# Optimization experiments

Measured on AMD Instinct MI355X. Metric: run time of the kernel, lower is better.

## Reference

```python
import jax, jax.numpy as jnp
import numpy as np

B, S, D, H = 4, 2048, 768, 12
HD = D // H  # head_dim = 64

def setup_inputs() -> dict:
    key = jax.random.key(0)
    k1, k2, k3 = jax.random.split(key, 3)
    scale = 0.02
    return {
        "x": jax.random.normal(k1, (B, S, D), dtype=jnp.float32),
        "w_qkv": jax.random.normal(k2, (D, 3 * D), dtype=jnp.float32) * scale,
        "b_qkv": jnp.zeros((3 * D,), dtype=jnp.float32),
        "w_proj": jax.random.normal(k3, (D, D), dtype=jnp.float32) * scale,
        "b_proj": jnp.zeros((D,), dtype=jnp.float32),
    }

def reference(x, w_qkv, b_qkv, w_proj, b_proj):
    b, s, d = x.shape
    hd = d // H
    attn_scale = hd ** -0.5
    qkv = x @ w_qkv + b_qkv                      # [b, s, 3d]
    qkv = qkv.reshape(b, s, 3, H, hd)
    q, k, v = jnp.moveaxis(qkv, 2, 0)            # each [b, s, H, hd]
    q = q.transpose(0, 2, 1, 3)                  # [b, H, s, hd]
    k = k.transpose(0, 2, 1, 3)
    v = v.transpose(0, 2, 1, 3)
    attn = jnp.einsum("bhqd,bhkd->bhqk", q, k) * attn_scale  # [b, H, s, s]
    causal = jnp.tril(jnp.ones((s, s), dtype=bool))
    attn = jnp.where(causal[None, None], attn, -jnp.inf)
    attn = jax.nn.softmax(attn, axis=-1)
    out = jnp.einsum("bhqk,bhkd->bhqd", attn, v)  # [b, H, s, hd]
    out = out.transpose(0, 2, 1, 3).reshape(b, s, d)
    return out @ w_proj + b_proj
```

## Files before the change

### kernel.cpp

```cpp
#include <hip/hip_runtime.h>
#include <hip/hip_bf16.h>
#include <cstdint>

typedef __bf16 bf16_t;
typedef __bf16 bf16x4 __attribute__((ext_vector_type(4)));
typedef __bf16 bf16x8 __attribute__((ext_vector_type(8)));
typedef float floatx4 __attribute__((ext_vector_type(4)));
typedef float floatx16 __attribute__((ext_vector_type(16)));
typedef unsigned int u32x4 __attribute__((ext_vector_type(4)));

#define NB 4
#define NH 12
#define SEQ 2048
#define DM 768
#define LOG2E 1.44269504088896340736f

__device__ __forceinline__ void gload_lds16(const bf16_t* g, bf16_t* l) {
  auto gp = reinterpret_cast<const __attribute__((address_space(1))) uint32_t*>(
      reinterpret_cast<uintptr_t>(g));
  auto lp = reinterpret_cast<__attribute__((address_space(3))) uint32_t*>(
      reinterpret_cast<uintptr_t>(l));
  __builtin_amdgcn_global_load_lds(gp, lp, 16, 0, 0);
}

__device__ __forceinline__ unsigned int pack2(float a, float b) {
  bf16_t x = (bf16_t)a, y = (bf16_t)b;
  unsigned short ux = __builtin_bit_cast(unsigned short, x);
  unsigned short uy = __builtin_bit_cast(unsigned short, y);
  return (unsigned int)ux | ((unsigned int)uy << 16);
}

__global__ __launch_bounds__(256) void prep_kernel(
    const float* __restrict__ x, bf16_t* __restrict__ xb,
    const float* __restrict__ wqkv, bf16_t* __restrict__ wqkvT,
    const float* __restrict__ wproj, bf16_t* __restrict__ wprojT) {
  const int bid = blockIdx.x;
  const int tid = threadIdx.x;
  if (bid < 6144) {
    int i = (bid * 256 + tid) * 4;
    float4 v = *(const float4*)(x + i);
    bf16x4 hh;
    hh[0] = (bf16_t)v.x; hh[1] = (bf16_t)v.y; hh[2] = (bf16_t)v.z; hh[3] = (bf16_t)v.w;
    *(bf16x4*)(xb + i) = hh;
    return;
  }
  const float* in;
  bf16_t* out;
  int N, nb, kb;
  if (bid < 7872) {
    int t = bid - 6144;
    in = wqkv; out = wqkvT; N = 2304;
    nb = (t % 72) * 32; kb = (t / 72) * 32;
  } else {
    int t = bid - 7872;
    in = wproj; out = wprojT; N = 768;
    nb = (t % 24) * 32; kb = (t / 24) * 32;
  }
  const int K = 768;
  __shared__ float tile[32][33];
  int tx = tid & 31, ty = tid >> 5;
#pragma unroll
  for (int r = ty; r < 32; r += 8)
    tile[r][tx] = in[(size_t)(kb + r) * N + nb + tx];
  __syncthreads();
#pragma unroll
  for (int r = ty; r < 32; r += 8)
    out[(size_t)(nb + r) * K + kb + tx] = (bf16_t)tile[tx][r];
}

__global__ __launch_bounds__(256) void gemm_qkv_kernel(
    const bf16_t* __restrict__ A, const bf16_t* __restrict__ BT,
    const float* __restrict__ bias,
    bf16_t* __restrict__ Qo, bf16_t* __restrict__ Ko, bf16_t* __restrict__ Vo) {
  const int K = 768;
  __shared__ __align__(16) bf16_t As[128][32];
  __shared__ __align__(16) bf16_t Bs[128][32];
  const int m0 = blockIdx.x * 128, n0 = blockIdx.y * 128;
  const int tid = threadIdx.x;
  const int w = tid >> 6, lane = tid & 63, quad = lane >> 4, l16 = lane & 15;
  const int wm = w >> 1, wn = w & 1;
  const int ldrow = w * 32;
  const int grow = lane >> 2;
  const int gcol = (lane & 3) * 8;

  floatx4 acc[4][4];
#pragma unroll
  for (int mt = 0; mt < 4; mt++)
#pragma unroll
    for (int nt = 0; nt < 4; nt++) acc[mt][nt] = (floatx4)(0.f);

  const bf16_t* ga0 = A + (size_t)(m0 + ldrow) * K;
  const bf16_t* gb0 = BT + (size_t)(n0 + ldrow) * K;

  for (int k0 = 0; k0 < K; k0 += 32) {
    __syncthreads();
    gload_lds16(ga0 + (size_t)grow * K + k0 + gcol,        &As[ldrow][0]);
    gload_lds16(ga0 + (size_t)(grow + 16) * K + k0 + gcol, &As[ldrow + 16][0]);
    gload_lds16(gb0 + (size_t)grow * K + k0 + gcol,        &Bs[ldrow][0]);
    gload_lds16(gb0 + (size_t)(grow + 16) * K + k0 + gcol, &Bs[ldrow + 16][0]);
    __syncthreads();
    bf16x8 af[4], bfr[4];
#pragma unroll
    for (int mt = 0; mt < 4; mt++)
      af[mt] = *(const bf16x8*)&As[wm * 64 + mt * 16 + l16][quad * 8];
#pragma unroll
    for (int nt = 0; nt < 4; nt++)
      bfr[nt] = *(const bf16x8*)&Bs[wn * 64 + nt * 16 + l16][quad * 8];
#pragma unroll
    for (int mt = 0; mt < 4; mt++)
#pragma unroll
      for (int nt = 0; nt < 4; nt++)
        acc[mt][nt] = __builtin_amdgcn_mfma_f32_16x16x32_bf16(af[mt], bfr[nt], acc[mt][nt], 0, 0, 0);
  }

  const int which = n0 / 768;
  const int rem0 = n0 % 768;
  bf16_t* dst = which == 0 ? Qo : (which == 1 ? Ko : Vo);
  const float qscale = which == 0 ? (0.125f * LOG2E) : 1.0f;
#pragma unroll
  for (int nt = 0; nt < 4; nt++) {
    const int cc = wn * 64 + nt * 16 + l16;
    const int rem = rem0 + cc;
    const int h = rem >> 6, hd = rem & 63;
    const float bv = bias[n0 + cc];
#pragma unroll
    for (int mt = 0; mt < 4; mt++)
#pragma unroll
      for (int r = 0; r < 4; r++) {
        const int gr = m0 + wm * 64 + mt * 16 + quad * 4 + r;
        const int bb = gr >> 11, s = gr & 2047;
        const float val = (acc[mt][nt][r] + bv) * qscale;
        dst[((size_t)((bb * NH + h) * SEQ + s)) * 64 + hd] = (bf16_t)val;
      }
  }
}

__global__ __launch_bounds__(256) void vtrans_kernel(const bf16_t* __restrict__ V,
                                                     bf16_t* __restrict__ Vt) {
  __shared__ bf16_t tile[64][66];
  int bh = blockIdx.y, s0 = blockIdx.x * 64;
  int tid = threadIdx.x;
  int r = tid >> 4, c4 = (tid & 15) * 4;
  const bf16_t* src = V + (size_t)bh * SEQ * 64;
#pragma unroll
  for (int rr = r; rr < 64; rr += 16)
    *(bf16x4*)&tile[rr][c4] = *(const bf16x4*)&src[(size_t)(s0 + rr) * 64 + c4];
  __syncthreads();
  bf16_t* dst = Vt + (size_t)bh * 64 * SEQ;
#pragma unroll
  for (int hd = r; hd < 64; hd += 16) {
    bf16x4 o;
    o[0] = tile[c4 + 0][hd]; o[1] = tile[c4 + 1][hd];
    o[2] = tile[c4 + 2][hd]; o[3] = tile[c4 + 3][hd];
    *(bf16x4*)&dst[(size_t)hd * SEQ + s0 + c4] = o;
  }
}

__global__ __launch_bounds__(512, 4) void attn_kernel(
    const bf16_t* __restrict__ Q, const bf16_t* __restrict__ Kg,
    const bf16_t* __restrict__ Vt, bf16_t* __restrict__ Out) {
  __shared__ __align__(16) bf16_t Ks[3][64 * 64];
  __shared__ __align__(16) bf16_t Vs[3][64 * 64];
  const int tid = threadIdx.x;
  const int w = tid >> 6, lane = tid & 63;
  const int l31 = lane & 31, hi = lane >> 5;
  const int bh = blockIdx.x;
  const int b = bh / NH, h = bh % NH;
  const int qt = (int)(gridDim.y - 1) - (int)blockIdx.y;
  const int r0 = qt * 256 + w * 32;
  const int qrow = r0 + l31;
  const bf16_t* Qp = Q + (size_t)bh * SEQ * 64;
  const bf16_t* Kp = Kg + (size_t)bh * SEQ * 64;
  const bf16_t* Vp = Vt + (size_t)bh * 64 * SEQ;

  bf16x8 qf[4];
#pragma unroll
  for (int kc = 0; kc < 4; kc++)
    qf[kc] = *(const bf16x8*)&Qp[(size_t)qrow * 64 + kc * 16 + hi * 8];

  bf16x8 ones;
#pragma unroll
  for (int j = 0; j < 8; j++) ones[j] = (bf16_t)1.0f;

  float m_i = -1e30f;
  floatx16 accT[2];
  accT[0] = (floatx16)(0.f);
  accT[1] = (floatx16)(0.f);
  floatx16 zl = (floatx16)(0.f);

  const int nt_w = (r0 >> 6) + 1;
  const int ntmax = 4 * qt + 4;

  const int srow = tid >> 3;
  const int scolb = ((tid & 7) ^ (srow & 7)) << 4;

  auto stage = [&](int buf, int kt) {
    const int kbase = kt * 64;
    gload_lds16(Kp + (size_t)(kbase + srow) * 64 + (scolb >> 1), &Ks[buf][w * 512]);
    gload_lds16(Vp + (size_t)srow * SEQ + kbase + (scolb >> 1), &Vs[buf][w * 512]);
  };

  const int swz = (l31 & 7) << 4;

  stage(0, 0);

  int cur = 0;
  for (int kt = 0; kt < ntmax; kt++) {
    const int nxt = (cur == 2) ? 0 : cur + 1;
    if (kt + 1 < ntmax) {
      stage(nxt, kt + 1);
      asm volatile("s_waitcnt vmcnt(2)" ::: "memory");
    } else {
      asm volatile("s_waitcnt vmcnt(0)" ::: "memory");
    }
    __builtin_amdgcn_s_barrier();

    if (kt < nt_w) {
      const int kbase = kt * 64;
      const bf16_t* Kb = Ks[cur];
      const bf16_t* Vb = Vs[cur];
      floatx16 st[2];
#pragma unroll
      for (int kt2 = 0; kt2 < 2; kt2++) {
        const int row = kt2 * 32 + l31;
        floatx16 z = (floatx16)(0.f);
#pragma unroll
        for (int kc = 0; kc < 4; kc++) {
          bf16x8 kfr = *(const bf16x8*)&Kb[row * 64 + (((kc * 32 + hi * 16) ^ swz) >> 1)];
          z = __builtin_amdgcn_mfma_f32_32x32x16_bf16(kfr, qf[kc], z, 0, 0, 0);
        }
        st[kt2] = z;
      }
      if (kt == nt_w - 1) {
#pragma unroll
        for (int kt2 = 0; kt2 < 2; kt2++)
#pragma unroll
          for (int r = 0; r < 16; r++) {
            int key = kbase + kt2 * 32 + (r & 3) + 8 * (r >> 2) + 4 * hi;
            if (key > qrow) st[kt2][r] = -1e30f;
          }
      }
      float mloc = -1e30f;
#pragma unroll
      for (int kt2 = 0; kt2 < 2; kt2++)
#pragma unroll
        for (int r = 0; r < 16; r++) mloc = fmaxf(mloc, st[kt2][r]);
      mloc = fmaxf(mloc, __shfl_xor(mloc, 32));
      if (!__all((int)(mloc - m_i <= 8.f))) {
        const float mnew = fmaxf(m_i, mloc);
        const float al = __builtin_amdgcn_exp2f(m_i - mnew);
        m_i = mnew;
#pragma unroll
        for (int r = 0; r < 16; r++) zl[r] *= al;
#pragma unroll
        for (int dt = 0; dt < 2; dt++)
#pragma unroll
          for (int r = 0; r < 16; r++) accT[dt][r] *= al;
      }
#pragma unroll
      for (int kt2 = 0; kt2 < 2; kt2++)
#pragma unroll
        for (int r = 0; r < 16; r++)
          st[kt2][r] = __builtin_amdgcn_exp2f(st[kt2][r] - m_i);
#pragma unroll
      for (int kt2 = 0; kt2 < 2; kt2++) {
        unsigned int wds[8];
#pragma unroll
        for (int j = 0; j < 8; j++) wds[j] = pack2(st[kt2][2 * j], st[kt2][2 * j + 1]);
        unsigned int x0 = (unsigned int)__shfl_xor((int)(hi ? wds[0] : wds[2]), 32);
        unsigned int x1 = (unsigned int)__shfl_xor((int)(hi ? wds[1] : wds[3]), 32);
        unsigned int x2 = (unsigned int)__shfl_xor((int)(hi ? wds[4] : wds[6]), 32);
        unsigned int x3 = (unsigned int)__shfl_xor((int)(hi ? wds[5] : wds[7]), 32);
        u32x4 f0 = hi ? (u32x4){x0, x1, wds[2], wds[3]} : (u32x4){wds[0], wds[1], x0, x1};
        u32x4 f1 = hi ? (u32x4){x2, x3, wds[6], wds[7]} : (u32x4){wds[4], wds[5], x2, x3};
        bf16x8 pf0 = __builtin_bit_cast(bf16x8, f0);
        bf16x8 pf1 = __builtin_bit_cast(bf16x8, f1);
        zl = __builtin_amdgcn_mfma_f32_32x32x16_bf16(ones, pf0, zl, 0, 0, 0);
        zl = __builtin_amdgcn_mfma_f32_32x32x16_bf16(ones, pf1, zl, 0, 0, 0);
#pragma unroll
        for (int dt = 0; dt < 2; dt++) {
          const int vrow = dt * 32 + l31;
          bf16x8 v0 = *(const bf16x8*)&Vb[vrow * 64 + (((kt2 * 64 + hi * 16) ^ swz) >> 1)];
          bf16x8 v1 = *(const bf16x8*)&Vb[vrow * 64 + (((kt2 * 64 + 32 + hi * 16) ^ swz) >> 1)];
          accT[dt] = __builtin_amdgcn_mfma_f32_32x32x16_bf16(v0, pf0, accT[dt], 0, 0, 0);
          accT[dt] = __builtin_amdgcn_mfma_f32_32x32x16_bf16(v1, pf1, accT[dt], 0, 0, 0);
        }
      }
    }
    cur = nxt;
  }

  const float inv_l = 1.0f / zl[0];
#pragma unroll
  for (int dt = 0; dt < 2; dt++)
#pragma unroll
    for (int g = 0; g < 4; g++) {
      bf16x4 o;
#pragma unroll
      for (int j = 0; j < 4; j++) o[j] = (bf16_t)(accT[dt][4 * g + j] * inv_l);
      int d = dt * 32 + 8 * g + 4 * hi;
      *(bf16x4*)&Out[((size_t)(b * SEQ + qrow)) * DM + h * 64 + d] = o;
    }
}

__global__ __launch_bounds__(256) void gemm_proj_kernel(
    const bf16_t* __restrict__ A, const bf16_t* __restrict__ BT,
    const float* __restrict__ bias, float* __restrict__ out) {
  const int K = 768;
  __shared__ __align__(16) bf16_t As[128][32];
  __shared__ __align__(16) bf16_t Bs[128][32];
  const int m0 = blockIdx.x * 128, n0 = blockIdx.y * 128;
  const int tid = threadIdx.x;
  const int w = tid >> 6, lane = tid & 63, quad = lane >> 4, l16 = lane & 15;
  const int wm = w >> 1, wn = w & 1;
  const int ldrow = w * 32;
  const int grow = lane >> 2;
  const int gcol = (lane & 3) * 8;

  floatx4 acc[4][4];
#pragma unroll
  for (int mt = 0; mt < 4; mt++)
#pragma unroll
    for (int nt = 0; nt < 4; nt++) acc[mt][nt] = (floatx4)(0.f);

  const bf16_t* ga0 = A + (size_t)(m0 + ldrow) * K;
  const bf16_t* gb0 = BT + (size_t)(n0 + ldrow) * K;

  for (int k0 = 0; k0 < K; k0 += 32) {
    __syncthreads();
    gload_lds16(ga0 + (size_t)grow * K + k0 + gcol,        &As[ldrow][0]);
    gload_lds16(ga0 + (size_t)(grow + 16) * K + k0 + gcol, &As[ldrow + 16][0]);
    gload_lds16(gb0 + (size_t)grow * K + k0 + gcol,        &Bs[ldrow][0]);
    gload_lds16(gb0 + (size_t)(grow + 16) * K + k0 + gcol, &Bs[ldrow + 16][0]);
    __syncthreads();
    bf16x8 af[4], bfr[4];
#pragma unroll
    for (int mt = 0; mt < 4; mt++)
      af[mt] = *(const bf16x8*)&As[wm * 64 + mt * 16 + l16][quad * 8];
#pragma unroll
    for (int nt = 0; nt < 4; nt++)
      bfr[nt] = *(const bf16x8*)&Bs[wn * 64 + nt * 16 + l16][quad * 8];
#pragma unroll
    for (int mt = 0; mt < 4; mt++)
#pragma unroll
      for (int nt = 0; nt < 4; nt++)
        acc[mt][nt] = __builtin_amdgcn_mfma_f32_16x16x32_bf16(af[mt], bfr[nt], acc[mt][nt], 0, 0, 0);
  }

#pragma unroll
  for (int nt = 0; nt < 4; nt++) {
    const int gc = n0 + wn * 64 + nt * 16 + l16;
    const float bv = bias[gc];
#pragma unroll
    for (int mt = 0; mt < 4; mt++)
#pragma unroll
      for (int r = 0; r < 4; r++) {
        const int gr = m0 + wm * 64 + mt * 16 + quad * 4 + r;
        out[(size_t)gr * 768 + gc] = acc[mt][nt][r] + bv;
      }
  }
}

extern "C" void kernel_launch(void* const* d_in, const int* in_sizes, int n_in,
                              void* d_out, int out_size, void* d_ws, size_t ws_size,
                              hipStream_t stream) {
  const float* x      = (const float*)d_in[0];
  const float* w_qkv  = (const float*)d_in[1];
  const float* b_qkv  = (const float*)d_in[2];
  const float* w_proj = (const float*)d_in[3];
  const float* b_proj = (const float*)d_in[4];
  float* out = (float*)d_out;
  char* ws = (char*)d_ws;

  bf16_t* xb     = (bf16_t*)(ws + 0);
  bf16_t* wqkvT  = (bf16_t*)(ws + 12582912);
  bf16_t* wprojT = (bf16_t*)(ws + 16121856);
  bf16_t* q      = (bf16_t*)(ws + 17301504);
  bf16_t* k      = (bf16_t*)(ws + 29884416);
  bf16_t* v      = (bf16_t*)(ws + 42467328);
  bf16_t* ao     = (bf16_t*)(ws + 55050240);
  bf16_t* vt     = xb;

  prep_kernel<<<8448, 256, 0, stream>>>(x, xb, w_qkv, wqkvT, w_proj, wprojT);
  gemm_qkv_kernel<<<dim3(64, 18), 256, 0, stream>>>(xb, wqkvT, b_qkv, q, k, v);
  vtrans_kernel<<<dim3(32, 48), 256, 0, stream>>>(v, vt);
  attn_kernel<<<dim3(48, 8), 512, 0, stream>>>(q, k, vt, ao);
  gemm_proj_kernel<<<dim3(64, 6), 256, 0, stream>>>(ao, wprojT, b_proj, out);
}
```

Baseline: 214.5 us.

## Triple-buffer GEMM K-loop loads and halve attention query tile per block

```diff
diff --git a/kernel.cpp b/kernel.cpp
--- a/kernel.cpp
+++ b/kernel.cpp
@@ -73,8 +73,9 @@
     const float* __restrict__ bias,
     bf16_t* __restrict__ Qo, bf16_t* __restrict__ Ko, bf16_t* __restrict__ Vo) {
   const int K = 768;
-  __shared__ __align__(16) bf16_t As[128][32];
-  __shared__ __align__(16) bf16_t Bs[128][32];
+  const int NT = 24;
+  __shared__ __align__(16) bf16_t As[3][128 * 32];
+  __shared__ __align__(16) bf16_t Bs[3][128 * 32];
   const int m0 = blockIdx.x * 128, n0 = blockIdx.y * 128;
   const int tid = threadIdx.x;
   const int w = tid >> 6, lane = tid & 63, quad = lane >> 4, l16 = lane & 15;
@@ -92,25 +93,38 @@
   const bf16_t* ga0 = A + (size_t)(m0 + ldrow) * K;
   const bf16_t* gb0 = BT + (size_t)(n0 + ldrow) * K;
 
-  for (int k0 = 0; k0 < K; k0 += 32) {
-    __syncthreads();
-    gload_lds16(ga0 + (size_t)grow * K + k0 + gcol,        &As[ldrow][0]);
-    gload_lds16(ga0 + (size_t)(grow + 16) * K + k0 + gcol, &As[ldrow + 16][0]);
-    gload_lds16(gb0 + (size_t)grow * K + k0 + gcol,        &Bs[ldrow][0]);
-    gload_lds16(gb0 + (size_t)(grow + 16) * K + k0 + gcol, &Bs[ldrow + 16][0]);
-    __syncthreads();
+  auto stage = [&](int buf, int k0) {
+    gload_lds16(ga0 + (size_t)grow * K + k0 + gcol,        &As[buf][ldrow * 32]);
+    gload_lds16(ga0 + (size_t)(grow + 16) * K + k0 + gcol, &As[buf][(ldrow + 16) * 32]);
+    gload_lds16(gb0 + (size_t)grow * K + k0 + gcol,        &Bs[buf][ldrow * 32]);
+    gload_lds16(gb0 + (size_t)(grow + 16) * K + k0 + gcol, &Bs[buf][(ldrow + 16) * 32]);
+  };
+
+  stage(0, 0);
+  int cur = 0;
+  for (int t = 0; t < NT; t++) {
+    const int nxt = (cur == 2) ? 0 : cur + 1;
+    if (t + 1 < NT) {
+      stage(nxt, (t + 1) * 32);
+      asm volatile("s_waitcnt vmcnt(4)" ::: "memory");
+    } else {
+      asm volatile("s_waitcnt vmcnt(0)" ::: "memory");
+    }
+    __builtin_amdgcn_s_barrier();
+
     bf16x8 af[4], bfr[4];
 #pragma unroll
     for (int mt = 0; mt < 4; mt++)
-      af[mt] = *(const bf16x8*)&As[wm * 64 + mt * 16 + l16][quad * 8];
+      af[mt] = *(const bf16x8*)&As[cur][(wm * 64 + mt * 16 + l16) * 32 + quad * 8];
 #pragma unroll
     for (int nt = 0; nt < 4; nt++)
-      bfr[nt] = *(const bf16x8*)&Bs[wn * 64 + nt * 16 + l16][quad * 8];
+      bfr[nt] = *(const bf16x8*)&Bs[cur][(wn * 64 + nt * 16 + l16) * 32 + quad * 8];
 #pragma unroll
     for (int mt = 0; mt < 4; mt++)
 #pragma unroll
       for (int nt = 0; nt < 4; nt++)
         acc[mt][nt] = __builtin_amdgcn_mfma_f32_16x16x32_bf16(af[mt], bfr[nt], acc[mt][nt], 0, 0, 0);
+    cur = nxt;
   }
 
   const int which = n0 / 768;
@@ -156,7 +170,7 @@
   }
 }
 
-__global__ __launch_bounds__(512, 4) void attn_kernel(
+__global__ __launch_bounds__(256, 3) void attn_kernel(
     const bf16_t* __restrict__ Q, const bf16_t* __restrict__ Kg,
     const bf16_t* __restrict__ Vt, bf16_t* __restrict__ Out) {
   __shared__ __align__(16) bf16_t Ks[3][64 * 64];
@@ -167,7 +181,7 @@
   const int bh = blockIdx.x;
   const int b = bh / NH, h = bh % NH;
   const int qt = (int)(gridDim.y - 1) - (int)blockIdx.y;
-  const int r0 = qt * 256 + w * 32;
+  const int r0 = qt * 128 + w * 32;
   const int qrow = r0 + l31;
   const bf16_t* Qp = Q + (size_t)bh * SEQ * 64;
   const bf16_t* Kp = Kg + (size_t)bh * SEQ * 64;
@@ -189,15 +203,26 @@
   floatx16 zl = (floatx16)(0.f);
 
   const int nt_w = (r0 >> 6) + 1;
-  const int ntmax = 4 * qt + 4;
-
-  const int srow = tid >> 3;
-  const int scolb = ((tid & 7) ^ (srow & 7)) << 4;
+  const int ntmax = 2 * qt + 2;
+
+  int srow[2], scolb[2];
+#pragma unroll
+  for (int r = 0; r < 2; r++) {
+    int off = r * 4096 + w * 1024 + lane * 16;
+    int row = off >> 7;
+    srow[r] = row;
+    scolb[r] = (off & 127) ^ ((row & 7) << 4);
+  }
 
   auto stage = [&](int buf, int kt) {
     const int kbase = kt * 64;
-    gload_lds16(Kp + (size_t)(kbase + srow) * 64 + (scolb >> 1), &Ks[buf][w * 512]);
-    gload_lds16(Vp + (size_t)srow * SEQ + kbase + (scolb >> 1), &Vs[buf][w * 512]);
+#pragma unroll
+    for (int r = 0; r < 2; r++) {
+      gload_lds16(Kp + (size_t)(kbase + srow[r]) * 64 + (scolb[r] >> 1),
+                  &Ks[buf][r * 2048 + w * 512]);
+      gload_lds16(Vp + (size_t)srow[r] * SEQ + kbase + (scolb[r] >> 1),
+                  &Vs[buf][r * 2048 + w * 512]);
+    }
   };
 
   const int swz = (l31 & 7) << 4;
@@ -209,7 +234,7 @@
     const int nxt = (cur == 2) ? 0 : cur + 1;
     if (kt + 1 < ntmax) {
       stage(nxt, kt + 1);
-      asm volatile("s_waitcnt vmcnt(2)" ::: "memory");
+      asm volatile("s_waitcnt vmcnt(4)" ::: "memory");
     } else {
       asm volatile("s_waitcnt vmcnt(0)" ::: "memory");
     }
@@ -307,8 +332,9 @@
     const bf16_t* __restrict__ A, const bf16_t* __restrict__ BT,
     const float* __restrict__ bias, float* __restrict__ out) {
   const int K = 768;
-  __shared__ __align__(16) bf16_t As[128][32];
-  __shared__ __align__(16) bf16_t Bs[128][32];
+  const int NT = 24;
+  __shared__ __align__(16) bf16_t As[3][128 * 32];
+  __shared__ __align__(16) bf16_t Bs[3][128 * 32];
   const int m0 = blockIdx.x * 128, n0 = blockIdx.y * 128;
   const int tid = threadIdx.x;
   const int w = tid >> 6, lane = tid & 63, quad = lane >> 4, l16 = lane & 15;
@@ -326,25 +352,38 @@
   const bf16_t* ga0 = A + (size_t)(m0 + ldrow) * K;
   const bf16_t* gb0 = BT + (size_t)(n0 + ldrow) * K;
 
-  for (int k0 = 0; k0 < K; k0 += 32) {
-    __syncthreads();
-    gload_lds16(ga0 + (size_t)grow * K + k0 + gcol,        &As[ldrow][0]);
-    gload_lds16(ga0 + (size_t)(grow + 16) * K + k0 + gcol, &As[ldrow + 16][0]);
-    gload_lds16(gb0 + (size_t)grow * K + k0 + gcol,        &Bs[ldrow][0]);
-    gload_lds16(gb0 + (size_t)(grow + 16) * K + k0 + gcol, &Bs[ldrow + 16][0]);
-    __syncthreads();
+  auto stage = [&](int buf, int k0) {
+    gload_lds16(ga0 + (size_t)grow * K + k0 + gcol,        &As[buf][ldrow * 32]);
+    gload_lds16(ga0 + (size_t)(grow + 16) * K + k0 + gcol, &As[buf][(ldrow + 16) * 32]);
+    gload_lds16(gb0 + (size_t)grow * K + k0 + gcol,        &Bs[buf][ldrow * 32]);
+    gload_lds16(gb0 + (size_t)(grow + 16) * K + k0 + gcol, &Bs[buf][(ldrow + 16) * 32]);
+  };
+
+  stage(0, 0);
+  int cur = 0;
+  for (int t = 0; t < NT; t++) {
+    const int nxt = (cur == 2) ? 0 : cur + 1;
+    if (t + 1 < NT) {
+      stage(nxt, (t + 1) * 32);
+      asm volatile("s_waitcnt vmcnt(4)" ::: "memory");
+    } else {
+      asm volatile("s_waitcnt vmcnt(0)" ::: "memory");
+    }
+    __builtin_amdgcn_s_barrier();
+
     bf16x8 af[4], bfr[4];
 #pragma unroll
     for (int mt = 0; mt < 4; mt++)
-      af[mt] = *(const bf16x8*)&As[wm * 64 + mt * 16 + l16][quad * 8];
+      af[mt] = *(const bf16x8*)&As[cur][(wm * 64 + mt * 16 + l16) * 32 + quad * 8];
 #pragma unroll
     for (int nt = 0; nt < 4; nt++)
-      bfr[nt] = *(const bf16x8*)&Bs[wn * 64 + nt * 16 + l16][quad * 8];
+      bfr[nt] = *(const bf16x8*)&Bs[cur][(wn * 64 + nt * 16 + l16) * 32 + quad * 8];
 #pragma unroll
     for (int mt = 0; mt < 4; mt++)
 #pragma unroll
       for (int nt = 0; nt < 4; nt++)
         acc[mt][nt] = __builtin_amdgcn_mfma_f32_16x16x32_bf16(af[mt], bfr[nt], acc[mt][nt], 0, 0, 0);
+    cur = nxt;
   }
 
 #pragma unroll
@@ -384,6 +423,6 @@
   prep_kernel<<<8448, 256, 0, stream>>>(x, xb, w_qkv, wqkvT, w_proj, wprojT);
   gemm_qkv_kernel<<<dim3(64, 18), 256, 0, stream>>>(xb, wqkvT, b_qkv, q, k, v);
   vtrans_kernel<<<dim3(32, 48), 256, 0, stream>>>(v, vt);
-  attn_kernel<<<dim3(48, 8), 512, 0, stream>>>(q, k, vt, ao);
+  attn_kernel<<<dim3(48, 16), 256, 0, stream>>>(q, k, vt, ao);
   gemm_proj_kernel<<<dim3(64, 6), 256, 0, stream>>>(ao, wprojT, b_proj, out);
 }
```

After: 205.9 us. 1.04x faster.

## Fuse V transpose into QKV GEMM epilogue and shrink attention blocks to 64 query rows

Applied to the files above, without the earlier changes.

```diff
diff --git a/kernel.cpp b/kernel.cpp
--- a/kernel.cpp
+++ b/kernel.cpp
@@ -71,10 +71,11 @@
 __global__ __launch_bounds__(256) void gemm_qkv_kernel(
     const bf16_t* __restrict__ A, const bf16_t* __restrict__ BT,
     const float* __restrict__ bias,
-    bf16_t* __restrict__ Qo, bf16_t* __restrict__ Ko, bf16_t* __restrict__ Vo) {
+    bf16_t* __restrict__ Qo, bf16_t* __restrict__ Ko, bf16_t* __restrict__ Vto) {
   const int K = 768;
-  __shared__ __align__(16) bf16_t As[128][32];
-  __shared__ __align__(16) bf16_t Bs[128][32];
+  __shared__ __align__(16) bf16_t smem[128 * 136];
+  bf16_t* As = smem;
+  bf16_t* Bs = smem + 4096;
   const int m0 = blockIdx.x * 128, n0 = blockIdx.y * 128;
   const int tid = threadIdx.x;
   const int w = tid >> 6, lane = tid & 63, quad = lane >> 4, l16 = lane & 15;
@@ -94,18 +95,18 @@
 
   for (int k0 = 0; k0 < K; k0 += 32) {
     __syncthreads();
-    gload_lds16(ga0 + (size_t)grow * K + k0 + gcol,        &As[ldrow][0]);
-    gload_lds16(ga0 + (size_t)(grow + 16) * K + k0 + gcol, &As[ldrow + 16][0]);
-    gload_lds16(gb0 + (size_t)grow * K + k0 + gcol,        &Bs[ldrow][0]);
-    gload_lds16(gb0 + (size_t)(grow + 16) * K + k0 + gcol, &Bs[ldrow + 16][0]);
+    gload_lds16(ga0 + (size_t)grow * K + k0 + gcol,        &As[ldrow * 32]);
+    gload_lds16(ga0 + (size_t)(grow + 16) * K + k0 + gcol, &As[(ldrow + 16) * 32]);
+    gload_lds16(gb0 + (size_t)grow * K + k0 + gcol,        &Bs[ldrow * 32]);
+    gload_lds16(gb0 + (size_t)(grow + 16) * K + k0 + gcol, &Bs[(ldrow + 16) * 32]);
     __syncthreads();
     bf16x8 af[4], bfr[4];
 #pragma unroll
     for (int mt = 0; mt < 4; mt++)
-      af[mt] = *(const bf16x8*)&As[wm * 64 + mt * 16 + l16][quad * 8];
+      af[mt] = *(const bf16x8*)&As[(wm * 64 + mt * 16 + l16) * 32 + quad * 8];
 #pragma unroll
     for (int nt = 0; nt < 4; nt++)
-      bfr[nt] = *(const bf16x8*)&Bs[wn * 64 + nt * 16 + l16][quad * 8];
+      bfr[nt] = *(const bf16x8*)&Bs[(wn * 64 + nt * 16 + l16) * 32 + quad * 8];
 #pragma unroll
     for (int mt = 0; mt < 4; mt++)
 #pragma unroll
@@ -115,59 +116,64 @@
 
   const int which = n0 / 768;
   const int rem0 = n0 % 768;
-  bf16_t* dst = which == 0 ? Qo : (which == 1 ? Ko : Vo);
-  const float qscale = which == 0 ? (0.125f * LOG2E) : 1.0f;
-#pragma unroll
-  for (int nt = 0; nt < 4; nt++) {
-    const int cc = wn * 64 + nt * 16 + l16;
-    const int rem = rem0 + cc;
+  if (which < 2) {
+    bf16_t* dst = which == 0 ? Qo : Ko;
+    const float qscale = which == 0 ? (0.125f * LOG2E) : 1.0f;
+#pragma unroll
+    for (int nt = 0; nt < 4; nt++) {
+      const int cc = wn * 64 + nt * 16 + l16;
+      const int rem = rem0 + cc;
+      const int h = rem >> 6, hd = rem & 63;
+      const float bv = bias[n0 + cc];
+#pragma unroll
+      for (int mt = 0; mt < 4; mt++)
+#pragma unroll
+        for (int r = 0; r < 4; r++) {
+          const int gr = m0 + wm * 64 + mt * 16 + quad * 4 + r;
+          const int bb = gr >> 11, s = gr & 2047;
+          const float val = (acc[mt][nt][r] + bv) * qscale;
+          dst[((size_t)((bb * NH + h) * SEQ + s)) * 64 + hd] = (bf16_t)val;
+        }
+    }
+  } else {
+    __syncthreads();
+#pragma unroll
+    for (int nt = 0; nt < 4; nt++) {
+      const int c = wn * 64 + nt * 16 + l16;
+      const float bv = bias[n0 + c];
+#pragma unroll
+      for (int mt = 0; mt < 4; mt++)
+#pragma unroll
+        for (int r = 0; r < 4; r++) {
+          const int grl = wm * 64 + mt * 16 + quad * 4 + r;
+          smem[c * 136 + grl] = (bf16_t)(acc[mt][nt][r] + bv);
+        }
+    }
+    __syncthreads();
+    const int c = tid >> 1, half = tid & 1;
+    const int rem = rem0 + c;
     const int h = rem >> 6, hd = rem & 63;
-    const float bv = bias[n0 + cc];
-#pragma unroll
-    for (int mt = 0; mt < 4; mt++)
-#pragma unroll
-      for (int r = 0; r < 4; r++) {
-        const int gr = m0 + wm * 64 + mt * 16 + quad * 4 + r;
-        const int bb = gr >> 11, s = gr & 2047;
-        const float val = (acc[mt][nt][r] + bv) * qscale;
-        dst[((size_t)((bb * NH + h) * SEQ + s)) * 64 + hd] = (bf16_t)val;
-      }
-  }
-}
-
-__global__ __launch_bounds__(256) void vtrans_kernel(const bf16_t* __restrict__ V,
-                                                     bf16_t* __restrict__ Vt) {
-  __shared__ bf16_t tile[64][66];
-  int bh = blockIdx.y, s0 = blockIdx.x * 64;
-  int tid = threadIdx.x;
-  int r = tid >> 4, c4 = (tid & 15) * 4;
-  const bf16_t* src = V + (size_t)bh * SEQ * 64;
-#pragma unroll
-  for (int rr = r; rr < 64; rr += 16)
-    *(bf16x4*)&tile[rr][c4] = *(const bf16x4*)&src[(size_t)(s0 + rr) * 64 + c4];
-  __syncthreads();
-  bf16_t* dst = Vt + (size_t)bh * 64 * SEQ;
-#pragma unroll
-  for (int hd = r; hd < 64; hd += 16) {
-    bf16x4 o;
-    o[0] = tile[c4 + 0][hd]; o[1] = tile[c4 + 1][hd];
-    o[2] = tile[c4 + 2][hd]; o[3] = tile[c4 + 3][hd];
-    *(bf16x4*)&dst[(size_t)hd * SEQ + s0 + c4] = o;
-  }
-}
-
-__global__ __launch_bounds__(512, 4) void attn_kernel(
+    const int bb = m0 >> 11;
+    const int s0 = (m0 & 2047) + half * 64;
+    bf16_t* dstp = Vto + (((size_t)(bb * NH + h) * 64 + hd) << 11) + s0;
+#pragma unroll
+    for (int j = 0; j < 8; j++)
+      *(bf16x8*)(dstp + j * 8) = *(const bf16x8*)&smem[c * 136 + half * 64 + j * 8];
+  }
+}
+
+__global__ __launch_bounds__(128, 3) void attn_kernel(
     const bf16_t* __restrict__ Q, const bf16_t* __restrict__ Kg,
     const bf16_t* __restrict__ Vt, bf16_t* __restrict__ Out) {
-  __shared__ __align__(16) bf16_t Ks[3][64 * 64];
-  __shared__ __align__(16) bf16_t Vs[3][64 * 64];
+  __shared__ __align__(16) bf16_t Ks[2][64 * 64];
+  __shared__ __align__(16) bf16_t Vs[2][64 * 64];
   const int tid = threadIdx.x;
   const int w = tid >> 6, lane = tid & 63;
   const int l31 = lane & 31, hi = lane >> 5;
   const int bh = blockIdx.x;
   const int b = bh / NH, h = bh % NH;
   const int qt = (int)(gridDim.y - 1) - (int)blockIdx.y;
-  const int r0 = qt * 256 + w * 32;
+  const int r0 = qt * 64 + w * 32;
   const int qrow = r0 + l31;
   const bf16_t* Qp = Q + (size_t)bh * SEQ * 64;
   const bf16_t* Kp = Kg + (size_t)bh * SEQ * 64;
@@ -188,16 +194,26 @@
   accT[1] = (floatx16)(0.f);
   floatx16 zl = (floatx16)(0.f);
 
-  const int nt_w = (r0 >> 6) + 1;
-  const int ntmax = 4 * qt + 4;
-
-  const int srow = tid >> 3;
-  const int scolb = ((tid & 7) ^ (srow & 7)) << 4;
+  const int ntmax = qt + 1;
+
+  int srow[4], scolb[4];
+#pragma unroll
+  for (int r = 0; r < 4; r++) {
+    int off = r * 2048 + tid * 16;
+    int row = off >> 7;
+    srow[r] = row;
+    scolb[r] = (off & 127) ^ ((row & 7) << 4);
+  }
 
   auto stage = [&](int buf, int kt) {
     const int kbase = kt * 64;
-    gload_lds16(Kp + (size_t)(kbase + srow) * 64 + (scolb >> 1), &Ks[buf][w * 512]);
-    gload_lds16(Vp + (size_t)srow * SEQ + kbase + (scolb >> 1), &Vs[buf][w * 512]);
+#pragma unroll
+    for (int r = 0; r < 4; r++) {
+      gload_lds16(Kp + (size_t)(kbase + srow[r]) * 64 + (scolb[r] >> 1),
+                  &Ks[buf][r * 1024 + w * 512]);
+      gload_lds16(Vp + (size_t)srow[r] * SEQ + kbase + (scolb[r] >> 1),
+                  &Vs[buf][r * 1024 + w * 512]);
+    }
   };
 
   const int swz = (l31 & 7) << 4;
@@ -206,16 +222,15 @@
 
   int cur = 0;
   for (int kt = 0; kt < ntmax; kt++) {
-    const int nxt = (cur == 2) ? 0 : cur + 1;
     if (kt + 1 < ntmax) {
-      stage(nxt, kt + 1);
-      asm volatile("s_waitcnt vmcnt(2)" ::: "memory");
+      stage(cur ^ 1, kt + 1);
+      asm volatile("s_waitcnt vmcnt(8)" ::: "memory");
     } else {
       asm volatile("s_waitcnt vmcnt(0)" ::: "memory");
     }
     __builtin_amdgcn_s_barrier();
 
-    if (kt < nt_w) {
+    {
       const int kbase = kt * 64;
       const bf16_t* Kb = Ks[cur];
       const bf16_t* Vb = Vs[cur];
@@ -231,7 +246,7 @@
         }
         st[kt2] = z;
       }
-      if (kt == nt_w - 1) {
+      if (kt == ntmax - 1) {
 #pragma unroll
         for (int kt2 = 0; kt2 < 2; kt2++)
 #pragma unroll
@@ -287,7 +302,8 @@
         }
       }
     }
-    cur = nxt;
+    __builtin_amdgcn_s_barrier();
+    cur ^= 1;
   }
 
   const float inv_l = 1.0f / zl[0];
@@ -377,13 +393,11 @@
   bf16_t* wprojT = (bf16_t*)(ws + 16121856);
   bf16_t* q      = (bf16_t*)(ws + 17301504);
   bf16_t* k      = (bf16_t*)(ws + 29884416);
-  bf16_t* v      = (bf16_t*)(ws + 42467328);
+  bf16_t* vt     = (bf16_t*)(ws + 42467328);
   bf16_t* ao     = (bf16_t*)(ws + 55050240);
-  bf16_t* vt     = xb;
 
   prep_kernel<<<8448, 256, 0, stream>>>(x, xb, w_qkv, wqkvT, w_proj, wprojT);
-  gemm_qkv_kernel<<<dim3(64, 18), 256, 0, stream>>>(xb, wqkvT, b_qkv, q, k, v);
-  vtrans_kernel<<<dim3(32, 48), 256, 0, stream>>>(v, vt);
-  attn_kernel<<<dim3(48, 8), 512, 0, stream>>>(q, k, vt, ao);
+  gemm_qkv_kernel<<<dim3(64, 18), 256, 0, stream>>>(xb, wqkvT, b_qkv, q, k, vt);
+  attn_kernel<<<dim3(48, 32), 128, 0, stream>>>(q, k, vt, ao);
   gemm_proj_kernel<<<dim3(64, 6), 256, 0, stream>>>(ao, wprojT, b_proj, out);
 }
```

After: 219.2 us. 1.02x slower.

## Enlarge QKV GEMM tiles with double-buffered swizzled LDS; shrink attention blocks

Applied to the files above, without the earlier changes.

```diff
diff --git a/kernel.cpp b/kernel.cpp
--- a/kernel.cpp
+++ b/kernel.cpp
@@ -68,49 +68,97 @@
     out[(size_t)(nb + r) * K + kb + tx] = (bf16_t)tile[tx][r];
 }
 
-__global__ __launch_bounds__(256) void gemm_qkv_kernel(
+__global__ __launch_bounds__(512, 2) void gemm_qkv_kernel(
     const bf16_t* __restrict__ A, const bf16_t* __restrict__ BT,
     const float* __restrict__ bias,
     bf16_t* __restrict__ Qo, bf16_t* __restrict__ Ko, bf16_t* __restrict__ Vo) {
   const int K = 768;
-  __shared__ __align__(16) bf16_t As[128][32];
-  __shared__ __align__(16) bf16_t Bs[128][32];
-  const int m0 = blockIdx.x * 128, n0 = blockIdx.y * 128;
+  const int NKT = 12;
+  __shared__ __align__(16) bf16_t As[2][16384];
+  __shared__ __align__(16) bf16_t Bs[2][16384];
+  const int m0 = blockIdx.x * 256, n0 = blockIdx.y * 256;
   const int tid = threadIdx.x;
   const int w = tid >> 6, lane = tid & 63, quad = lane >> 4, l16 = lane & 15;
-  const int wm = w >> 1, wn = w & 1;
-  const int ldrow = w * 32;
-  const int grow = lane >> 2;
-  const int gcol = (lane & 3) * 8;
-
-  floatx4 acc[4][4];
-#pragma unroll
-  for (int mt = 0; mt < 4; mt++)
-#pragma unroll
-    for (int nt = 0; nt < 4; nt++) acc[mt][nt] = (floatx4)(0.f);
-
-  const bf16_t* ga0 = A + (size_t)(m0 + ldrow) * K;
-  const bf16_t* gb0 = BT + (size_t)(n0 + ldrow) * K;
-
-  for (int k0 = 0; k0 < K; k0 += 32) {
-    __syncthreads();
-    gload_lds16(ga0 + (size_t)grow * K + k0 + gcol,        &As[ldrow][0]);
-    gload_lds16(ga0 + (size_t)(grow + 16) * K + k0 + gcol, &As[ldrow + 16][0]);
-    gload_lds16(gb0 + (size_t)grow * K + k0 + gcol,        &Bs[ldrow][0]);
-    gload_lds16(gb0 + (size_t)(grow + 16) * K + k0 + gcol, &Bs[ldrow + 16][0]);
-    __syncthreads();
-    bf16x8 af[4], bfr[4];
-#pragma unroll
-    for (int mt = 0; mt < 4; mt++)
-      af[mt] = *(const bf16x8*)&As[wm * 64 + mt * 16 + l16][quad * 8];
-#pragma unroll
-    for (int nt = 0; nt < 4; nt++)
-      bfr[nt] = *(const bf16x8*)&Bs[wn * 64 + nt * 16 + l16][quad * 8];
-#pragma unroll
-    for (int mt = 0; mt < 4; mt++)
-#pragma unroll
-      for (int nt = 0; nt < 4; nt++)
-        acc[mt][nt] = __builtin_amdgcn_mfma_f32_16x16x32_bf16(af[mt], bfr[nt], acc[mt][nt], 0, 0, 0);
+  const int wm = w >> 2, wn = w & 3;
+  const int swz = (l16 & 7) << 4;
+
+  floatx4 acc[8][4];
+#pragma unroll
+  for (int m = 0; m < 8; m++)
+#pragma unroll
+    for (int n = 0; n < 4; n++) acc[m][n] = (floatx4)(0.f);
+
+  int srow[2], scol[2];
+#pragma unroll
+  for (int j = 0; j < 2; j++) {
+    int off = j * 8192 + tid * 16;
+    int row = off >> 7;
+    srow[j] = row;
+    scol[j] = (((off & 127) ^ ((row & 7) << 4)) >> 1);
+  }
+
+  auto stageA = [&](int d, int h, int kt) {
+#pragma unroll
+    for (int j = 0; j < 2; j++)
+      gload_lds16(A + (size_t)(m0 + h * 128 + srow[j]) * K + kt * 64 + scol[j],
+                  &As[d][h * 8192 + j * 4096 + w * 512]);
+  };
+  auto stageB = [&](int d, int h, int kt) {
+#pragma unroll
+    for (int j = 0; j < 2; j++)
+      gload_lds16(BT + (size_t)(n0 + h * 128 + srow[j]) * K + kt * 64 + scol[j],
+                  &Bs[d][h * 8192 + j * 4096 + w * 512]);
+  };
+
+  stageA(0, 0, 0); stageB(0, 0, 0); stageA(0, 1, 0); stageB(0, 1, 0);
+
+  for (int kt = 0; kt < NKT; kt++) {
+    const int d = kt & 1, nd = d ^ 1;
+    asm volatile("s_waitcnt vmcnt(0)" ::: "memory");
+    __builtin_amdgcn_s_barrier();
+
+    bf16x8 bf[4][2];
+#pragma unroll
+    for (int p = 0; p < 4; p++) {
+      bf16x8 af[2][2];
+#pragma unroll
+      for (int mi = 0; mi < 2; mi++) {
+        const int ri = p * 32 + mi * 16 + l16;
+#pragma unroll
+        for (int kk = 0; kk < 2; kk++)
+          af[mi][kk] = *(const bf16x8*)&As[d][wm * 8192 + ri * 64 +
+                                             (((kk * 64 + quad * 16) ^ swz) >> 1)];
+      }
+      if (p == 0) {
+#pragma unroll
+        for (int n = 0; n < 4; n++) {
+          const int row = wn * 64 + n * 16 + l16;
+          const int h = row >> 7, ri = row & 127;
+#pragma unroll
+          for (int kk = 0; kk < 2; kk++)
+            bf[n][kk] = *(const bf16x8*)&Bs[d][h * 8192 + ri * 64 +
+                                              (((kk * 64 + quad * 16) ^ swz) >> 1)];
+        }
+      }
+      if (p < 2 && kt + 1 < NKT) {
+        stageA(nd, p, kt + 1);
+        stageB(nd, p, kt + 1);
+      }
+      __builtin_amdgcn_s_barrier();
+      asm volatile("s_waitcnt lgkmcnt(0)" ::: "memory");
+      __builtin_amdgcn_sched_barrier(0);
+      __builtin_amdgcn_s_setprio(1);
+#pragma unroll
+      for (int mi = 0; mi < 2; mi++)
+#pragma unroll
+        for (int n = 0; n < 4; n++)
+#pragma unroll
+          for (int kk = 0; kk < 2; kk++)
+            acc[p * 2 + mi][n] = __builtin_amdgcn_mfma_f32_16x16x32_bf16(
+                af[mi][kk], bf[n][kk], acc[p * 2 + mi][n], 0, 0, 0);
+      __builtin_amdgcn_s_setprio(0);
+      if (p < 3) __builtin_amdgcn_s_barrier();
+    }
   }
 
   const int which = n0 / 768;
@@ -118,18 +166,18 @@
   bf16_t* dst = which == 0 ? Qo : (which == 1 ? Ko : Vo);
   const float qscale = which == 0 ? (0.125f * LOG2E) : 1.0f;
 #pragma unroll
-  for (int nt = 0; nt < 4; nt++) {
-    const int cc = wn * 64 + nt * 16 + l16;
+  for (int n = 0; n < 4; n++) {
+    const int cc = wn * 64 + n * 16 + l16;
     const int rem = rem0 + cc;
     const int h = rem >> 6, hd = rem & 63;
     const float bv = bias[n0 + cc];
 #pragma unroll
-    for (int mt = 0; mt < 4; mt++)
+    for (int m = 0; m < 8; m++)
 #pragma unroll
       for (int r = 0; r < 4; r++) {
-        const int gr = m0 + wm * 64 + mt * 16 + quad * 4 + r;
+        const int gr = m0 + wm * 128 + m * 16 + quad * 4 + r;
         const int bb = gr >> 11, s = gr & 2047;
-        const float val = (acc[mt][nt][r] + bv) * qscale;
+        const float val = (acc[m][n][r] + bv) * qscale;
         dst[((size_t)((bb * NH + h) * SEQ + s)) * 64 + hd] = (bf16_t)val;
       }
   }
@@ -156,7 +204,7 @@
   }
 }
 
-__global__ __launch_bounds__(512, 4) void attn_kernel(
+__global__ __launch_bounds__(256, 3) void attn_kernel(
     const bf16_t* __restrict__ Q, const bf16_t* __restrict__ Kg,
     const bf16_t* __restrict__ Vt, bf16_t* __restrict__ Out) {
   __shared__ __align__(16) bf16_t Ks[3][64 * 64];
@@ -167,7 +215,7 @@
   const int bh = blockIdx.x;
   const int b = bh / NH, h = bh % NH;
   const int qt = (int)(gridDim.y - 1) - (int)blockIdx.y;
-  const int r0 = qt * 256 + w * 32;
+  const int r0 = qt * 128 + w * 32;
   const int qrow = r0 + l31;
   const bf16_t* Qp = Q + (size_t)bh * SEQ * 64;
   const bf16_t* Kp = Kg + (size_t)bh * SEQ * 64;
@@ -189,15 +237,26 @@
   floatx16 zl = (floatx16)(0.f);
 
   const int nt_w = (r0 >> 6) + 1;
-  const int ntmax = 4 * qt + 4;
-
-  const int srow = tid >> 3;
-  const int scolb = ((tid & 7) ^ (srow & 7)) << 4;
+  const int ntmax = 2 * qt + 2;
+
+  int srow[2], scolb[2];
+#pragma unroll
+  for (int r = 0; r < 2; r++) {
+    int off = r * 4096 + w * 1024 + lane * 16;
+    int row = off >> 7;
+    srow[r] = row;
+    scolb[r] = (off & 127) ^ ((row & 7) << 4);
+  }
 
   auto stage = [&](int buf, int kt) {
     const int kbase = kt * 64;
-    gload_lds16(Kp + (size_t)(kbase + srow) * 64 + (scolb >> 1), &Ks[buf][w * 512]);
-    gload_lds16(Vp + (size_t)srow * SEQ + kbase + (scolb >> 1), &Vs[buf][w * 512]);
+#pragma unroll
+    for (int r = 0; r < 2; r++) {
+      gload_lds16(Kp + (size_t)(kbase + srow[r]) * 64 + (scolb[r] >> 1),
+                  &Ks[buf][r * 2048 + w * 512]);
+      gload_lds16(Vp + (size_t)srow[r] * SEQ + kbase + (scolb[r] >> 1),
+                  &Vs[buf][r * 2048 + w * 512]);
+    }
   };
 
   const int swz = (l31 & 7) << 4;
@@ -209,7 +268,7 @@
     const int nxt = (cur == 2) ? 0 : cur + 1;
     if (kt + 1 < ntmax) {
       stage(nxt, kt + 1);
-      asm volatile("s_waitcnt vmcnt(2)" ::: "memory");
+      asm volatile("s_waitcnt vmcnt(4)" ::: "memory");
     } else {
       asm volatile("s_waitcnt vmcnt(0)" ::: "memory");
     }
@@ -382,8 +441,8 @@
   bf16_t* vt     = xb;
 
   prep_kernel<<<8448, 256, 0, stream>>>(x, xb, w_qkv, wqkvT, w_proj, wprojT);
-  gemm_qkv_kernel<<<dim3(64, 18), 256, 0, stream>>>(xb, wqkvT, b_qkv, q, k, v);
+  gemm_qkv_kernel<<<dim3(32, 9), 512, 0, stream>>>(xb, wqkvT, b_qkv, q, k, v);
   vtrans_kernel<<<dim3(32, 48), 256, 0, stream>>>(v, vt);
-  attn_kernel<<<dim3(48, 8), 512, 0, stream>>>(q, k, vt, ao);
+  attn_kernel<<<dim3(48, 16), 256, 0, stream>>>(q, k, vt, ao);
   gemm_proj_kernel<<<dim3(64, 6), 256, 0, stream>>>(ao, wprojT, b_proj, out);
 }
```

Measured after the change: 216.8 us. No clear change (+1.1%).
